# Kernel optimization log

Measured on AMD Instinct MI355X. Metric: run time of the kernel, lower is better.

## Reference

```python
import jax, jax.numpy as jnp
import numpy as np

B, T, D, H, L, W = 32, 512, 256, 8, 2, 10
NQ = 10000
HD = D // H


def setup_inputs():
    key = jax.random.key(0)
    ks = jax.random.split(key, 16)
    def n(k, shape, s=0.02):
        return jax.random.normal(k, shape, jnp.float32) * s
    return {
        "q": jax.random.randint(ks[0], (B, T), 0, NQ),
        "s": jax.random.randint(ks[1], (B, T), 0, 2),
        "q_embed": n(ks[2], (NQ + 1, D)),
        "s_embed": n(ks[3], (2, D)),
        "pos_embed": n(ks[4], (512, D)),
        "fusion_w": n(ks[5], (2 * D, D)),
        "fusion_b": jnp.zeros((D,), jnp.float32),
        "in_proj_w": n(ks[6], (L, D, 3 * D)),
        "in_proj_b": jnp.zeros((L, 3 * D), jnp.float32),
        "out_proj_w": n(ks[7], (L, D, D)),
        "out_proj_b": jnp.zeros((L, D), jnp.float32),
        "ln1_g": jnp.ones((L, D), jnp.float32),
        "ln1_b": jnp.zeros((L, D), jnp.float32),
        "ln2_g": jnp.ones((L, D), jnp.float32),
        "ln2_b": jnp.zeros((L, D), jnp.float32),
        "ff1_w": n(ks[8], (L, D, 4 * D)),
        "ff1_b": jnp.zeros((L, 4 * D), jnp.float32),
        "ff2_w": n(ks[9], (L, 4 * D, D)),
        "ff2_b": jnp.zeros((L, D), jnp.float32),
        "sw1": n(ks[10], (6, 32), 0.1),
        "sb1": jnp.zeros((32,), jnp.float32),
        "sw2": n(ks[11], (32, D // 4), 0.1),
        "sb2": jnp.zeros((D // 4,), jnp.float32),
        "cw1": n(ks[12], (D + D // 4, D)),
        "cb1": jnp.zeros((D,), jnp.float32),
        "cw2": n(ks[13], (D, 1)),
        "cb2": jnp.zeros((1,), jnp.float32),
    }


def _ln(x, g, b):
    mu = jnp.mean(x, -1, keepdims=True)
    var = jnp.mean(jnp.square(x - mu), -1, keepdims=True)
    return (x - mu) * jax.lax.rsqrt(var + 1e-5) * g + b


def _sliding_sum(x, w):
    # sum over trailing window of size w ending at each t, via prefix sums
    c = jnp.concatenate([jnp.zeros((x.shape[0], 1), x.dtype), jnp.cumsum(x, axis=1)], axis=1)
    t = jnp.arange(x.shape[1])
    return c[:, t + 1] - c[:, jnp.maximum(t + 1 - w, 0)]


def _stats(s, mask):
    # vectorized version of _extract_statistics (prefix-sum sliding windows)
    mf = mask.astype(jnp.float32)
    sf = s.astype(jnp.float32) * mf
    valid = _sliding_sum(mf, W)
    correct_rate = _sliding_sum(sf, W) / (valid + 1e-6)
    rc = _sliding_sum(mf, 5)
    recent_correct = _sliding_sum(sf, 5) / (rc + 1e-6)
    trans = ((s[:, 1:] != s[:, :-1]) & mask[:, 1:] & mask[:, :-1]).astype(jnp.float32)
    diff = jnp.concatenate([jnp.zeros((s.shape[0], 1), jnp.float32), trans], axis=1)
    change_rate = _sliding_sum(diff, W - 1) / (valid + 1e-6)
    # max consecutive equal run within each trailing window of size W
    sp = jnp.pad(s, ((0, 0), (W - 1, 0)))
    mp = jnp.pad(mask, ((0, 0), (W - 1, 0)))
    win_s = [sp[:, j:j + T] for j in range(W)]
    win_m = [mp[:, j:j + T] for j in range(W)]
    run = win_m[0].astype(jnp.float32)
    mx = run
    for j in range(1, W):  # fixed small window, not a data-dim loop
        eq = (win_s[j] == win_s[j - 1]) & win_m[j - 1]
        run = win_m[j].astype(jnp.float32) * (jnp.where(eq, run, 0.0) + 1.0)
        mx = jnp.maximum(mx, run)
    rel = jnp.broadcast_to(jnp.arange(T, dtype=jnp.float32) / max(T, 100), s.shape)
    cov = valid / W
    return jnp.stack([correct_rate, recent_correct, change_rate, mx / W, rel, cov], axis=-1)


def reference(q, s, q_embed, s_embed, pos_embed, fusion_w, fusion_b, in_proj_w, in_proj_b,
              out_proj_w, out_proj_b, ln1_g, ln1_b, ln2_g, ln2_b, ff1_w, ff1_b, ff2_w, ff2_b,
              sw1, sb1, sw2, sb2, cw1, cb1, cw2, cb2):
    mask = s >= 0
    qm = jnp.where(mask, q, 0)
    sm = jnp.where(mask, s, 0)
    h = jnp.concatenate([q_embed[qm], s_embed[sm]], axis=-1)  # [B,T,2D]
    h = jax.nn.relu(h @ fusion_w + fusion_b) + pos_embed[:T][None]
    causal = jnp.tril(jnp.ones((T, T), bool))
    allowed = causal[None, None] & mask[:, None, None, :]
    scale = 1.0 / (HD ** 0.5)
    for l in range(L):
        qkv = h @ in_proj_w[l] + in_proj_b[l]
        qh, kh, vh = jnp.split(qkv, 3, axis=-1)
        qh = qh.reshape(B, T, H, HD).transpose(0, 2, 1, 3)
        kh = kh.reshape(B, T, H, HD).transpose(0, 2, 1, 3)
        vh = vh.reshape(B, T, H, HD).transpose(0, 2, 1, 3)
        scores = jnp.einsum('bhqd,bhkd->bhqk', qh, kh) * scale
        scores = jnp.where(allowed, scores, -1e9)
        attn = jax.nn.softmax(scores, axis=-1)
        o = jnp.einsum('bhqk,bhkd->bhqd', attn, vh).transpose(0, 2, 1, 3).reshape(B, T, D)
        h = _ln(h + (o @ out_proj_w[l] + out_proj_b[l]), ln1_g[l], ln1_b[l])
        ff = jax.nn.gelu(h @ ff1_w[l] + ff1_b[l], approximate=False) @ ff2_w[l] + ff2_b[l]
        h = _ln(h + ff, ln2_g[l], ln2_b[l])
    sfeat = _stats(sm, mask)  # [B,T,6]
    semb = jax.nn.relu(sfeat @ sw1 + sb1) @ sw2 + sb2  # [B,T,D//4]
    comb = jnp.concatenate([h, semb], axis=-1)
    logits = (jax.nn.relu(comb @ cw1 + cb1) @ cw2 + cb2)[..., 0]
    return jnp.where(mask, logits, -1e9)
```

## Files before the change

kernel.cpp:

```cpp
#include <hip/hip_runtime.h>
#include <hip/hip_bf16.h>
#include <cmath>


using short8 = __attribute__((ext_vector_type(8))) short;
using short4v = __attribute__((ext_vector_type(4))) short;
using f32x4  = __attribute__((ext_vector_type(4))) float;

__device__ inline float gelu_f(float x) {
    return 0.5f * x * (1.0f + erff(x * 0.70710678118654752f));
}

__device__ inline short f2bf(float x) {
    union { float f; unsigned u; } v; v.f = x;
    return (short)((v.u + 0x7fffu + ((v.u >> 16) & 1u)) >> 16);
}

__device__ inline float bf2f(short v) {
    union { unsigned u; float f; } x; x.u = ((unsigned)(unsigned short)v) << 16;
    return x.f;
}

__device__ inline unsigned packbf(float lo, float hi) {
    union { float f; unsigned u; } a, b; a.f = lo; b.f = hi;
    unsigned ra = (a.u + 0x7fffu + ((a.u >> 16) & 1u)) >> 16;
    unsigned rb = (b.u + 0x7fffu + ((b.u >> 16) & 1u)) >> 16;
    return (rb << 16) | (ra & 0xffffu);
}

#define GLOAD16(gp, lp) __builtin_amdgcn_global_load_lds( \
    (const __attribute__((address_space(1))) void*)(gp), \
    (__attribute__((address_space(3))) void*)(lp), 16, 0, 0)

__global__ __launch_bounds__(256) void prep(
    const float* __restrict__ fusion_w, const float* __restrict__ in_proj_w,
    const float* __restrict__ out_proj_w, const float* __restrict__ ff1_w,
    const float* __restrict__ ff2_w, const float* __restrict__ cw1,
    short* __restrict__ wts,
    const int* __restrict__ s,
    short* __restrict__ semb,
    const float* __restrict__ sw1, const float* __restrict__ sb1,
    const float* __restrict__ sw2, const float* __restrict__ sb2)
{
    __shared__ float tile[32][33];
    __shared__ float sv_sh[512];
    __shared__ float m_sh[512];
    __shared__ float sw2_sh[2048];

    if (blockIdx.x < 1744) {
        const int b0[10]      = {0,128,320,512,576,640,896,1152,1408,1664};
        const int Ks[10]      = {512,256,256,256,256,256,256,1024,1024,320};
        const int Ns[10]      = {256,768,768,256,256,1024,1024,256,256,256};
        const int sidx[10]    = {0,1,1,2,2,3,3,4,4,5};
        const size_t soff[10] = {0,0,196608,0,65536,0,262144,0,262144,0};
        const size_t doff[10] = {0,131072,327680,524288,589824,655360,917504,1179648,1441792,1703936};
        const float* srcs[6] = {fusion_w, in_proj_w, out_proj_w, ff1_w, ff2_w, cw1};
        int bid = blockIdx.x;
        int mi = 0;
        while (mi < 9 && bid >= b0[mi + 1]) ++mi;
        int bl = bid - b0[mi];
        int K = Ks[mi], N = Ns[mi];
        int tx = bl % (N >> 5), ty = bl / (N >> 5);
        const float* src = srcs[sidx[mi]] + soff[mi];
        short* dst = wts + doff[mi];
        int c = threadIdx.x & 31, r = threadIdx.x >> 5;
#pragma unroll
        for (int i = 0; i < 4; ++i)
            tile[r + i * 8][c] = src[(size_t)(ty * 32 + r + i * 8) * N + tx * 32 + c];
        __syncthreads();
#pragma unroll
        for (int i = 0; i < 4; ++i)
            dst[(size_t)(tx * 32 + r + i * 8) * K + ty * 32 + c] = f2bf(tile[c][r + i * 8]);
    } else {
        const int b = blockIdx.x - 1744;
        const int tt = threadIdx.x;
        for (int t = tt; t < 512; t += 256) {
            int sval = s[b * 512 + t];
            bool mk = sval >= 0;
            sv_sh[t] = mk ? (float)sval : 0.f;
            m_sh[t] = mk ? 1.f : 0.f;
        }
        for (int i = tt; i < 2048; i += 256) sw2_sh[i] = sw2[i];
        __syncthreads();
        for (int half = 0; half < 2; ++half) {
            const int t = tt + half * 256;
            float mf10 = 0, sf10 = 0, mf5 = 0, sf5 = 0, d9 = 0;
#pragma unroll
            for (int k = 0; k < 10; ++k) {
                int idx = t - k;
                if (idx >= 0) {
                    float mv = m_sh[idx], sv = sv_sh[idx];
                    mf10 += mv; sf10 += sv;
                    if (k < 5) { mf5 += mv; sf5 += sv; }
                    if (k < 9 && idx >= 1) {
                        if (sv != sv_sh[idx - 1] && mv > 0.5f && m_sh[idx - 1] > 0.5f) d9 += 1.f;
                    }
                }
            }
            float run, mx;
            {
                int x0 = t - 9;
                run = (x0 >= 0) ? m_sh[x0] : 0.f;
                mx = run;
#pragma unroll
                for (int j = 1; j < 10; ++j) {
                    int xc = t + j - 9, xp = xc - 1;
                    float sc = (xc >= 0) ? sv_sh[xc] : 0.f;
                    float sp = (xp >= 0) ? sv_sh[xp] : 0.f;
                    float mc = (xc >= 0) ? m_sh[xc] : 0.f;
                    float mp = (xp >= 0) ? m_sh[xp] : 0.f;
                    bool eq = (sc == sp) && (mp > 0.5f);
                    run = (mc > 0.5f) ? ((eq ? run : 0.f) + 1.f) : 0.f;
                    mx = fmaxf(mx, run);
                }
            }
            float f[6];
            f[0] = sf10 / (mf10 + 1e-6f);
            f[1] = sf5 / (mf5 + 1e-6f);
            f[2] = d9 / (mf10 + 1e-6f);
            f[3] = mx * 0.1f;
            f[4] = (float)t * (1.f / 512.f);
            f[5] = mf10 * 0.1f;

            float hid[32];
#pragma unroll
            for (int j2 = 0; j2 < 32; ++j2) {
                float a = sb1[j2];
#pragma unroll
                for (int i = 0; i < 6; ++i) a = fmaf(f[i], sw1[i * 32 + j2], a);
                hid[j2] = fmaxf(a, 0.f);
            }
            short* orow = semb + ((size_t)b * 512 + t) * 64;
            for (int c = 0; c < 64; c += 4) {
                float v0 = sb2[c], v1 = sb2[c + 1], v2 = sb2[c + 2], v3 = sb2[c + 3];
#pragma unroll
                for (int j2 = 0; j2 < 32; ++j2) {
                    float hh = hid[j2];
                    v0 = fmaf(hh, sw2_sh[j2 * 64 + c], v0);
                    v1 = fmaf(hh, sw2_sh[j2 * 64 + c + 1], v1);
                    v2 = fmaf(hh, sw2_sh[j2 * 64 + c + 2], v2);
                    v3 = fmaf(hh, sw2_sh[j2 * 64 + c + 3], v3);
                }
                short4v o; o[0] = f2bf(v0); o[1] = f2bf(v1); o[2] = f2bf(v2); o[3] = f2bf(v3);
                *(short4v*)(orow + c) = o;
            }
        }
    }
}

template<int EPI, int KTOT>
__global__ __launch_bounds__(512) void kbs(
    const short* __restrict__ A, const short* __restrict__ A2,
    const short* __restrict__ Wt, const float* __restrict__ bias,
    short* __restrict__ o0, short* __restrict__ o1, short* __restrict__ o2,
    short* __restrict__ xbb, short* __restrict__ hb,
    const float* __restrict__ pos, const float* __restrict__ cw2v,
    float* __restrict__ pbuf,
    const int* __restrict__ qi, const int* __restrict__ si,
    const float* __restrict__ qe, const float* __restrict__ se)
{
    constexpr int BN = 64;
    constexpr int NCH = (KTOT + 255) / 256;
    constexpr int KA = (EPI == 4) ? 256 : KTOT;
    __shared__ short Bs[BN * 256];
    const int tid = threadIdx.x, lane = tid & 63, wv = tid >> 6;
    const int lg = lane >> 4, lr = lane & 15;
    const int n0 = blockIdx.y * BN;
    const int row0 = blockIdx.x * 128 + wv * 16;

    f32x4 acc[4] = {};
    short8 af[8];

#pragma unroll
    for (int c = 0; c < NCH; ++c) {
        const int ck = (KTOT - c * 256 >= 256) ? 256 : (KTOT - c * 256);
        const int spr = ck >> 3;
        if (c) __syncthreads();
        for (int i = 0; i < (BN * ck) / 8; i += 512) {
            int slot = i + tid;
            int n = slot / spr, posn = slot % spr;
            int g = posn ^ (n & 7);
            GLOAD16(Wt + (size_t)(n0 + n) * KTOT + c * 256 + g * 8, &Bs[slot * 8]);
        }
        const int nkk = ck >> 5;
        if constexpr (EPI == 0) {
            int row = row0 + lr;
            int sv = si[row];
            bool mk = sv >= 0;
            const float* base = (c == 0) ? qe + (size_t)(mk ? qi[row] : 0) * 256
                                         : se + (size_t)(mk ? sv : 0) * 256;
#pragma unroll
            for (int kk = 0; kk < 8; ++kk) {
                const float* p = base + kk * 32 + lg * 8;
                float4 v0 = *(const float4*)p;
                float4 v1 = *(const float4*)(p + 4);
                short8 o;
                o[0] = f2bf(v0.x); o[1] = f2bf(v0.y); o[2] = f2bf(v0.z); o[3] = f2bf(v0.w);
                o[4] = f2bf(v1.x); o[5] = f2bf(v1.y); o[6] = f2bf(v1.z); o[7] = f2bf(v1.w);
                af[kk] = o;
            }
        } else if (EPI == 4 && c == 1) {
            const short* ar2 = A2 + (size_t)(row0 + lr) * 64 + lg * 8;
            af[0] = *(const short8*)(ar2);
            af[1] = *(const short8*)(ar2 + 32);
        } else {
            const short* ar = A + (size_t)(row0 + lr) * KA + c * 256 + lg * 8;
#pragma unroll
            for (int kk = 0; kk < 8; ++kk)
                if (kk < nkk) af[kk] = *(const short8*)(ar + kk * 32);
        }
        __syncthreads();
#pragma unroll
        for (int kk = 0; kk < 8; ++kk) {
            if (kk >= nkk) break;
#pragma unroll
            for (int j = 0; j < 4; ++j) {
                int n = j * 16 + lr;
                short8 b = *(const short8*)&Bs[n * ck + (((kk * 4 + lg) ^ (n & 7)) << 3)];
                acc[j] = __builtin_amdgcn_mfma_f32_16x16x32_bf16(af[kk], b, acc[j], 0, 0, 0);
            }
        }
    }

    if constexpr (EPI == 0) {
#pragma unroll
        for (int j = 0; j < 4; ++j)
#pragma unroll
        for (int r = 0; r < 4; ++r) {
            int row = row0 + lg * 4 + r;
            int col = n0 + j * 16 + lr;
            float x = acc[j][r] + bias[col];
            x = fmaxf(x, 0.f) + pos[(size_t)(row & 511) * 256 + col];
            o0[(size_t)row * 256 + col] = f2bf(x);
        }
    } else if constexpr (EPI == 1) {
#pragma unroll
        for (int j = 0; j < 4; ++j)
#pragma unroll
        for (int r = 0; r < 4; ++r) {
            int row = row0 + lg * 4 + r;
            int gcol = n0 + j * 16 + lr;
            int t = row & 511, bg = row >> 9;
            int sec = gcol >> 8, cc = gcol & 255;
            int h = cc >> 5, d = cc & 31, bh = bg * 8 + h;
            short v = f2bf(acc[j][r] + bias[gcol]);
            if (sec == 0)      o0[((size_t)bh * 512 + t) * 32 + d] = v;
            else if (sec == 1) o1[((size_t)bh * 512 + t) * 32 + d] = v;
            else {
                int kl = t & 31;
                o2[(size_t)bh * 16384 + (size_t)(t >> 5) * 1024 +
                   (size_t)((kl >> 2) & 3) * 256 + d * 8 + (((kl & 3) << 1) | ((kl >> 4) & 1))] = v;
            }
        }
    } else if constexpr (EPI == 2) {
#pragma unroll
        for (int j = 0; j < 4; ++j)
#pragma unroll
        for (int r = 0; r < 4; ++r) {
            int row = row0 + lg * 4 + r;
            int gcol = n0 + j * 16 + lr;
            float x = acc[j][r] + bias[gcol];
            o0[(size_t)row * 1024 + gcol] = f2bf(gelu_f(x));
        }
    } else if constexpr (EPI == 3) {
#pragma unroll
        for (int j = 0; j < 4; ++j)
#pragma unroll
        for (int r = 0; r < 4; ++r) {
            int row = row0 + lg * 4 + r;
            int col = n0 + j * 16 + lr;
            xbb[(size_t)row * 256 + col] =
                f2bf(acc[j][r] + bias[col] + bf2f(hb[(size_t)row * 256 + col]));
        }
    } else {
#pragma unroll
        for (int r = 0; r < 4; ++r) {
            float p = 0.f;
#pragma unroll
            for (int j = 0; j < 4; ++j) {
                int col = n0 + j * 16 + lr;
                float v = fmaxf(acc[j][r] + bias[col], 0.f);
                p += v * cw2v[col];
            }
#pragma unroll
            for (int off = 1; off < 16; off <<= 1) p += __shfl_xor(p, off);
            if (lr == 0) {
                int row = row0 + lg * 4 + r;
                pbuf[(size_t)blockIdx.y * 16384 + row] = p;
            }
        }
    }
}

__global__ __launch_bounds__(256) void k_ln(
    const short* __restrict__ xbb, short* __restrict__ hb,
    const float* __restrict__ gamma, const float* __restrict__ beta)
{
    int row = blockIdx.x * 4 + (threadIdx.x >> 6);
    int lane = threadIdx.x & 63;
    int c = lane * 4;
    short4v xv4 = *(const short4v*)(xbb + (size_t)row * 256 + c);
    float x0 = bf2f(xv4[0]), x1 = bf2f(xv4[1]), x2 = bf2f(xv4[2]), x3 = bf2f(xv4[3]);
    float sm = x0 + x1 + x2 + x3;
    float sq = x0 * x0 + x1 * x1 + x2 * x2 + x3 * x3;
#pragma unroll
    for (int off = 32; off > 0; off >>= 1) {
        sm += __shfl_xor(sm, off);
        sq += __shfl_xor(sq, off);
    }
    float mu = sm * (1.f / 256.f);
    float var = sq * (1.f / 256.f) - mu * mu;
    float rstd = rsqrtf(var + 1e-5f);
    float4 gv = *reinterpret_cast<const float4*>(gamma + c);
    float4 bv = *reinterpret_cast<const float4*>(beta + c);
    short4v o;
    o[0] = f2bf((x0 - mu) * rstd * gv.x + bv.x);
    o[1] = f2bf((x1 - mu) * rstd * gv.y + bv.y);
    o[2] = f2bf((x2 - mu) * rstd * gv.z + bv.z);
    o[3] = f2bf((x3 - mu) * rstd * gv.w + bv.w);
    *(short4v*)(hb + (size_t)row * 256 + c) = o;
}

__global__ __launch_bounds__(256) void k_fin(
    const float* __restrict__ pbuf, const int* __restrict__ s,
    const float* __restrict__ cb2, float* __restrict__ out)
{
    int i = blockIdx.x * 256 + threadIdx.x;
    float v = pbuf[i] + pbuf[i + 16384] + pbuf[i + 32768] + pbuf[i + 49152] + cb2[0];
    out[i] = (s[i] >= 0) ? v : -1e9f;
}

__global__ __launch_bounds__(256) void attn_mfma(
    const short* __restrict__ Qg, const short* __restrict__ Kg,
    const short* __restrict__ VTg, short* __restrict__ O)
{
    __shared__ unsigned Wp[4][2][16][20];
    const int bh = blockIdx.x >> 2, part = blockIdx.x & 3;
    const int b = bh >> 3, h = bh & 7;
    const int wv = threadIdx.x >> 6, lane = threadIdx.x & 63;
    const int lg = lane >> 4, lr = lane & 15;
    const int slot = part * 4 + wv;
    const short* Qbh = Qg + (size_t)bh * 16384;
    const short* Kbh = Kg + (size_t)bh * 16384;
    const short* Vbh = VTg + (size_t)bh * 16384;
    const float scale = 0.17677669529663687f;

    const int tA = slot, tB = 31 - slot;
    const int qA0 = tA << 4, qB0 = tB << 4;
    const int nA = tA >> 1, nB = tB >> 1;
    short8 qaA = *(const short8*)(Qbh + (size_t)(qA0 + lr) * 32 + lg * 8);
    short8 qaB = *(const short8*)(Qbh + (size_t)(qB0 + lr) * 32 + lg * 8);
    f32x4 oA0 = {}, oA1 = {}, oB0 = {}, oB1 = {};
    float lA[4] = {0.f, 0.f, 0.f, 0.f};
    float lB[4] = {0.f, 0.f, 0.f, 0.f};

    auto chunk = [&](int c, int q0, int nfull, const short8& qa,
                     const short8& kf0, const short8& kf1,
                     const short8& vf0, const short8& vf1,
                     f32x4& o0, f32x4& o1, float* l_, int slab) {
        int kc = c << 5;
        f32x4 s0 = {}, s1 = {};
        s0 = __builtin_amdgcn_mfma_f32_16x16x32_bf16(qa, kf0, s0, 0, 0, 0);
        s1 = __builtin_amdgcn_mfma_f32_16x16x32_bf16(qa, kf1, s1, 0, 0, 0);
        float p0[4], p1[4];
        if (c < nfull) {
#pragma unroll
            for (int r = 0; r < 4; ++r) {
                p0[r] = __expf(s0[r] * scale);
                p1[r] = __expf(s1[r] * scale);
            }
        } else {
#pragma unroll
            for (int r = 0; r < 4; ++r) {
                int qq = q0 + lg * 4 + r;
                p0[r] = (kc + lr)      > qq ? 0.f : __expf(s0[r] * scale);
                p1[r] = (kc + 16 + lr) > qq ? 0.f : __expf(s1[r] * scale);
            }
        }
#pragma unroll
        for (int r = 0; r < 4; ++r) {
            l_[r] += p0[r] + p1[r];
            Wp[wv][slab][lg * 4 + r][lr] = packbf(p0[r], p1[r]);
        }
        short8 pa = *(const short8*)&Wp[wv][slab][lr][lg * 4];
        o0 = __builtin_amdgcn_mfma_f32_16x16x32_bf16(pa, vf0, o0, 0, 0, 0);
        o1 = __builtin_amdgcn_mfma_f32_16x16x32_bf16(pa, vf1, o1, 0, 0, 0);
    };

    int c = 0;
    for (; c <= nA; ++c) {
        int kc = c << 5;
        short8 kf0 = *(const short8*)(Kbh + (size_t)(kc + lr) * 32 + lg * 8);
        short8 kf1 = *(const short8*)(Kbh + (size_t)(kc + 16 + lr) * 32 + lg * 8);
        short8 vf0 = *(const short8*)(Vbh + (size_t)c * 1024 + lg * 256 + lr * 8);
        short8 vf1 = *(const short8*)(Vbh + (size_t)c * 1024 + lg * 256 + (lr + 16) * 8);
        chunk(c, qB0, nB, qaB, kf0, kf1, vf0, vf1, oB0, oB1, lB, 1);
        chunk(c, qA0, nA, qaA, kf0, kf1, vf0, vf1, oA0, oA1, lA, 0);
    }
    for (; c <= nB; ++c) {
        int kc = c << 5;
        short8 kf0 = *(const short8*)(Kbh + (size_t)(kc + lr) * 32 + lg * 8);
        short8 kf1 = *(const short8*)(Kbh + (size_t)(kc + 16 + lr) * 32 + lg * 8);
        short8 vf0 = *(const short8*)(Vbh + (size_t)c * 1024 + lg * 256 + lr * 8);
        short8 vf1 = *(const short8*)(Vbh + (size_t)c * 1024 + lg * 256 + (lr + 16) * 8);
        chunk(c, qB0, nB, qaB, kf0, kf1, vf0, vf1, oB0, oB1, lB, 1);
    }

#pragma unroll
    for (int off = 1; off < 16; off <<= 1)
#pragma unroll
        for (int r = 0; r < 4; ++r) {
            lA[r] += __shfl_xor(lA[r], off);
            lB[r] += __shfl_xor(lB[r], off);
        }
#pragma unroll
    for (int r = 0; r < 4; ++r) {
        float invA = 1.f / lA[r];
        size_t roA = ((size_t)b * 512 + qA0 + lg * 4 + r) * 256 + h * 32;
        O[roA + lr] = f2bf(oA0[r] * invA);
        O[roA + 16 + lr] = f2bf(oA1[r] * invA);
        float invB = 1.f / lB[r];
        size_t roB = ((size_t)b * 512 + qB0 + lg * 4 + r) * 256 + h * 32;
        O[roB + lr] = f2bf(oB0[r] * invB);
        O[roB + 16 + lr] = f2bf(oB1[r] * invB);
    }
}

extern "C" void kernel_launch(void* const* d_in, const int* in_sizes, int n_in,
                              void* d_out, int out_size, void* d_ws, size_t ws_size,
                              hipStream_t stream) {
    const int*   q         = (const int*)d_in[0];
    const int*   s         = (const int*)d_in[1];
    const float* q_embed   = (const float*)d_in[2];
    const float* s_embed   = (const float*)d_in[3];
    const float* pos_embed = (const float*)d_in[4];
    const float* fusion_w  = (const float*)d_in[5];
    const float* fusion_b  = (const float*)d_in[6];
    const float* in_proj_w = (const float*)d_in[7];
    const float* in_proj_b = (const float*)d_in[8];
    const float* out_proj_w= (const float*)d_in[9];
    const float* out_proj_b= (const float*)d_in[10];
    const float* ln1_g     = (const float*)d_in[11];
    const float* ln1_b     = (const float*)d_in[12];
    const float* ln2_g     = (const float*)d_in[13];
    const float* ln2_b     = (const float*)d_in[14];
    const float* ff1_w     = (const float*)d_in[15];
    const float* ff1_b     = (const float*)d_in[16];
    const float* ff2_w     = (const float*)d_in[17];
    const float* ff2_b     = (const float*)d_in[18];
    const float* sw1       = (const float*)d_in[19];
    const float* sb1       = (const float*)d_in[20];
    const float* sw2       = (const float*)d_in[21];
    const float* sb2       = (const float*)d_in[22];
    const float* cw1       = (const float*)d_in[23];
    const float* cb1       = (const float*)d_in[24];
    const float* cw2       = (const float*)d_in[25];
    const float* cb2       = (const float*)d_in[26];
    float* out = (float*)d_out;

    char* base = (char*)d_ws;
    short* hb   = (short*)(base);
    short* bufA = (short*)(base + 8388608);
    short* att  = (short*)(base + 41943040);
    short* Qg   = (short*)(base + 50331648);
    short* Kg   = (short*)(base + 58720256);
    short* VTg  = (short*)(base + 67108864);
    short* semb = (short*)(base + 75497472);
    short* wts  = (short*)(base + 77594624);
    short* xbb  = (short*)(base + 81166336);
    float* pbuf = (float*)(base + 89554944);

    const size_t W_FUSION = 0, W_INPROJ0 = 131072, W_INPROJ1 = 327680;
    const size_t W_OUTPROJ0 = 524288, W_OUTPROJ1 = 589824;
    const size_t W_FF1_0 = 655360, W_FF1_1 = 917504;
    const size_t W_FF2_0 = 1179648, W_FF2_1 = 1441792;
    const size_t W_CW1 = 1703936;

    prep<<<1776, 256, 0, stream>>>(fusion_w, in_proj_w, out_proj_w,
                                   ff1_w, ff2_w, cw1, wts,
                                   s, semb, sw1, sb1, sw2, sb2);
    kbs<0, 512><<<dim3(128, 4), 512, 0, stream>>>(nullptr, nullptr,
        wts + W_FUSION, fusion_b, hb, nullptr, nullptr, nullptr, nullptr,
        pos_embed, nullptr, nullptr, q, s, q_embed, s_embed);
    for (int l = 0; l < 2; ++l) {
        kbs<1, 256><<<dim3(128, 12), 512, 0, stream>>>(hb, nullptr,
            wts + (l ? W_INPROJ1 : W_INPROJ0), in_proj_b + l * 768,
            Qg, Kg, VTg, nullptr, nullptr, nullptr, nullptr, nullptr,
            nullptr, nullptr, nullptr, nullptr);
        attn_mfma<<<1024, 256, 0, stream>>>(Qg, Kg, VTg, att);
        kbs<3, 256><<<dim3(128, 4), 512, 0, stream>>>(att, nullptr,
            wts + (l ? W_OUTPROJ1 : W_OUTPROJ0), out_proj_b + l * 256,
            nullptr, nullptr, nullptr, xbb, hb, nullptr, nullptr, nullptr,
            nullptr, nullptr, nullptr, nullptr);
        k_ln<<<4096, 256, 0, stream>>>(xbb, hb, ln1_g + l * 256, ln1_b + l * 256);
        kbs<2, 256><<<dim3(128, 16), 512, 0, stream>>>(hb, nullptr,
            wts + (l ? W_FF1_1 : W_FF1_0), ff1_b + l * 1024,
            bufA, nullptr, nullptr, nullptr, nullptr, nullptr, nullptr, nullptr,
            nullptr, nullptr, nullptr, nullptr);
        kbs<3, 1024><<<dim3(128, 4), 512, 0, stream>>>(bufA, nullptr,
            wts + (l ? W_FF2_1 : W_FF2_0), ff2_b + l * 256,
            nullptr, nullptr, nullptr, xbb, hb, nullptr, nullptr, nullptr,
            nullptr, nullptr, nullptr, nullptr);
        k_ln<<<4096, 256, 0, stream>>>(xbb, hb, ln2_g + l * 256, ln2_b + l * 256);
    }
    kbs<4, 320><<<dim3(128, 4), 512, 0, stream>>>(hb, semb,
        wts + W_CW1, cb1, nullptr, nullptr, nullptr, nullptr, nullptr,
        nullptr, cw2, pbuf, nullptr, nullptr, nullptr, nullptr);
    k_fin<<<64, 256, 0, stream>>>(pbuf, s, cb2, out);
}
```

Baseline: 285.0 us.

## Fuse residual GEMMs with LayerNorm and classifier head into full-width kernels

Adds a kfull kernel in which each block computes all 256 output columns for 32 rows, so the residual add and LayerNorm can run in the GEMM epilogue through a cross-wave shared-memory reduction. This replaces the out-proj and FF2 GEMMs followed by separate k_ln launches, and also folds the classifier reduction and final masking into the head GEMM, removing k_fin and the xbb/pbuf intermediates. It removes several launches and round trips of intermediates through global memory. In exchange the grid shrinks to 512 blocks, and each block now stages the whole 256-column weight slab through shared memory in 128-wide K chunks.

```diff
diff --git a/kernel.cpp b/kernel.cpp
--- a/kernel.cpp
+++ b/kernel.cpp
@@ -150,18 +150,15 @@
 
 template<int EPI, int KTOT>
 __global__ __launch_bounds__(512) void kbs(
-    const short* __restrict__ A, const short* __restrict__ A2,
-    const short* __restrict__ Wt, const float* __restrict__ bias,
+    const short* __restrict__ A, const short* __restrict__ Wt,
+    const float* __restrict__ bias,
     short* __restrict__ o0, short* __restrict__ o1, short* __restrict__ o2,
-    short* __restrict__ xbb, short* __restrict__ hb,
-    const float* __restrict__ pos, const float* __restrict__ cw2v,
-    float* __restrict__ pbuf,
+    const float* __restrict__ pos,
     const int* __restrict__ qi, const int* __restrict__ si,
     const float* __restrict__ qe, const float* __restrict__ se)
 {
     constexpr int BN = 64;
     constexpr int NCH = (KTOT + 255) / 256;
-    constexpr int KA = (EPI == 4) ? 256 : KTOT;
     __shared__ short Bs[BN * 256];
     const int tid = threadIdx.x, lane = tid & 63, wv = tid >> 6;
     const int lg = lane >> 4, lr = lane & 15;
@@ -199,12 +196,8 @@
                 o[4] = f2bf(v1.x); o[5] = f2bf(v1.y); o[6] = f2bf(v1.z); o[7] = f2bf(v1.w);
                 af[kk] = o;
             }
-        } else if (EPI == 4 && c == 1) {
-            const short* ar2 = A2 + (size_t)(row0 + lr) * 64 + lg * 8;
-            af[0] = *(const short8*)(ar2);
-            af[1] = *(const short8*)(ar2 + 32);
         } else {
-            const short* ar = A + (size_t)(row0 + lr) * KA + c * 256 + lg * 8;
+            const short* ar = A + (size_t)(row0 + lr) * KTOT + c * 256 + lg * 8;
 #pragma unroll
             for (int kk = 0; kk < 8; ++kk)
                 if (kk < nkk) af[kk] = *(const short8*)(ar + kk * 32);
@@ -252,7 +245,7 @@
                    (size_t)((kl >> 2) & 3) * 256 + d * 8 + (((kl & 3) << 1) | ((kl >> 4) & 1))] = v;
             }
         }
-    } else if constexpr (EPI == 2) {
+    } else {
 #pragma unroll
         for (int j = 0; j < 4; ++j)
 #pragma unroll
@@ -262,72 +255,135 @@
             float x = acc[j][r] + bias[gcol];
             o0[(size_t)row * 1024 + gcol] = f2bf(gelu_f(x));
         }
-    } else if constexpr (EPI == 3) {
+    }
+}
+
+template<int EPI, int KTOT>
+__global__ __launch_bounds__(512) void kfull(
+    const short* __restrict__ A, const short* __restrict__ A2,
+    const short* __restrict__ Wt, const float* __restrict__ bias,
+    short* __restrict__ hb,
+    const float* __restrict__ gamma, const float* __restrict__ beta,
+    const float* __restrict__ cw2v, const float* __restrict__ cb2,
+    const int* __restrict__ smask, float* __restrict__ outlog)
+{
+    constexpr int NCH = (KTOT + 127) / 128;
+    constexpr int KA = (EPI == 1) ? 256 : KTOT;
+    __shared__ short Bs[256 * 128];
+    __shared__ float redS[32][4];
+    __shared__ float redQ[32][4];
+    const int tid = threadIdx.x, lane = tid & 63, wv = tid >> 6;
+    const int lg = lane >> 4, lr = lane & 15;
+    const int wr = wv >> 2, wc = wv & 3;
+    const int row0 = blockIdx.x * 32 + wr * 16;
+
+    f32x4 acc[4] = {};
+    short8 af[4];
+
+#pragma unroll
+    for (int c = 0; c < NCH; ++c) {
+        const int ck = (KTOT - c * 128 >= 128) ? 128 : (KTOT - c * 128);
+        const int spr = ck >> 3;
+        if (c) __syncthreads();
+        for (int i = 0; i < (256 * ck) / 8; i += 512) {
+            int slot = i + tid;
+            int n = slot / spr, posn = slot % spr;
+            int g = posn ^ (n & 7);
+            GLOAD16(Wt + (size_t)n * KTOT + c * 128 + g * 8, &Bs[slot * 8]);
+        }
+        const int nkk = ck >> 5;
+        if (EPI == 1 && c == 2) {
+            const short* ar2 = A2 + (size_t)(row0 + lr) * 64 + lg * 8;
+            af[0] = *(const short8*)(ar2);
+            af[1] = *(const short8*)(ar2 + 32);
+        } else {
+            const short* ar = A + (size_t)(row0 + lr) * KA + c * 128 + lg * 8;
+#pragma unroll
+            for (int kk = 0; kk < 4; ++kk)
+                if (kk < nkk) af[kk] = *(const short8*)(ar + kk * 32);
+        }
+        __syncthreads();
+#pragma unroll
+        for (int kk = 0; kk < 4; ++kk) {
+            if (kk >= nkk) break;
+#pragma unroll
+            for (int j = 0; j < 4; ++j) {
+                int n = wc * 64 + j * 16 + lr;
+                short8 b = *(const short8*)&Bs[n * ck + (((kk * 4 + lg) ^ (n & 7)) << 3)];
+                acc[j] = __builtin_amdgcn_mfma_f32_16x16x32_bf16(af[kk], b, acc[j], 0, 0, 0);
+            }
+        }
+    }
+
+    if constexpr (EPI == 0) {
+        float ps[4] = {0.f, 0.f, 0.f, 0.f}, pq[4] = {0.f, 0.f, 0.f, 0.f};
 #pragma unroll
         for (int j = 0; j < 4; ++j)
 #pragma unroll
         for (int r = 0; r < 4; ++r) {
             int row = row0 + lg * 4 + r;
-            int col = n0 + j * 16 + lr;
-            xbb[(size_t)row * 256 + col] =
-                f2bf(acc[j][r] + bias[col] + bf2f(hb[(size_t)row * 256 + col]));
+            int col = wc * 64 + j * 16 + lr;
+            float x = acc[j][r] + bias[col] + bf2f(hb[(size_t)row * 256 + col]);
+            acc[j][r] = x;
+            ps[r] += x; pq[r] += x * x;
+        }
+#pragma unroll
+        for (int off = 1; off < 16; off <<= 1)
+#pragma unroll
+            for (int r = 0; r < 4; ++r) {
+                ps[r] += __shfl_xor(ps[r], off);
+                pq[r] += __shfl_xor(pq[r], off);
+            }
+        if (lr == 0) {
+#pragma unroll
+            for (int r = 0; r < 4; ++r) {
+                int rl = wr * 16 + lg * 4 + r;
+                redS[rl][wc] = ps[r]; redQ[rl][wc] = pq[r];
+            }
+        }
+        __syncthreads();
+#pragma unroll
+        for (int r = 0; r < 4; ++r) {
+            int rl = wr * 16 + lg * 4 + r;
+            int row = row0 + lg * 4 + r;
+            float sm = redS[rl][0] + redS[rl][1] + redS[rl][2] + redS[rl][3];
+            float sq = redQ[rl][0] + redQ[rl][1] + redQ[rl][2] + redQ[rl][3];
+            float mu = sm * (1.f / 256.f);
+            float var = sq * (1.f / 256.f) - mu * mu;
+            float rstd = rsqrtf(var + 1e-5f);
+#pragma unroll
+            for (int j = 0; j < 4; ++j) {
+                int col = wc * 64 + j * 16 + lr;
+                float y = (acc[j][r] - mu) * rstd * gamma[col] + beta[col];
+                hb[(size_t)row * 256 + col] = f2bf(y);
+            }
         }
     } else {
-#pragma unroll
-        for (int r = 0; r < 4; ++r) {
-            float p = 0.f;
-#pragma unroll
-            for (int j = 0; j < 4; ++j) {
-                int col = n0 + j * 16 + lr;
-                float v = fmaxf(acc[j][r] + bias[col], 0.f);
-                p += v * cw2v[col];
-            }
-#pragma unroll
-            for (int off = 1; off < 16; off <<= 1) p += __shfl_xor(p, off);
-            if (lr == 0) {
-                int row = row0 + lg * 4 + r;
-                pbuf[(size_t)blockIdx.y * 16384 + row] = p;
-            }
-        }
-    }
-}
-
-__global__ __launch_bounds__(256) void k_ln(
-    const short* __restrict__ xbb, short* __restrict__ hb,
-    const float* __restrict__ gamma, const float* __restrict__ beta)
-{
-    int row = blockIdx.x * 4 + (threadIdx.x >> 6);
-    int lane = threadIdx.x & 63;
-    int c = lane * 4;
-    short4v xv4 = *(const short4v*)(xbb + (size_t)row * 256 + c);
-    float x0 = bf2f(xv4[0]), x1 = bf2f(xv4[1]), x2 = bf2f(xv4[2]), x3 = bf2f(xv4[3]);
-    float sm = x0 + x1 + x2 + x3;
-    float sq = x0 * x0 + x1 * x1 + x2 * x2 + x3 * x3;
-#pragma unroll
-    for (int off = 32; off > 0; off >>= 1) {
-        sm += __shfl_xor(sm, off);
-        sq += __shfl_xor(sq, off);
-    }
-    float mu = sm * (1.f / 256.f);
-    float var = sq * (1.f / 256.f) - mu * mu;
-    float rstd = rsqrtf(var + 1e-5f);
-    float4 gv = *reinterpret_cast<const float4*>(gamma + c);
-    float4 bv = *reinterpret_cast<const float4*>(beta + c);
-    short4v o;
-    o[0] = f2bf((x0 - mu) * rstd * gv.x + bv.x);
-    o[1] = f2bf((x1 - mu) * rstd * gv.y + bv.y);
-    o[2] = f2bf((x2 - mu) * rstd * gv.z + bv.z);
-    o[3] = f2bf((x3 - mu) * rstd * gv.w + bv.w);
-    *(short4v*)(hb + (size_t)row * 256 + c) = o;
-}
-
-__global__ __launch_bounds__(256) void k_fin(
-    const float* __restrict__ pbuf, const int* __restrict__ s,
-    const float* __restrict__ cb2, float* __restrict__ out)
-{
-    int i = blockIdx.x * 256 + threadIdx.x;
-    float v = pbuf[i] + pbuf[i + 16384] + pbuf[i + 32768] + pbuf[i + 49152] + cb2[0];
-    out[i] = (s[i] >= 0) ? v : -1e9f;
+        float p[4] = {0.f, 0.f, 0.f, 0.f};
+#pragma unroll
+        for (int j = 0; j < 4; ++j)
+#pragma unroll
+        for (int r = 0; r < 4; ++r) {
+            int col = wc * 64 + j * 16 + lr;
+            float v = fmaxf(acc[j][r] + bias[col], 0.f);
+            p[r] += v * cw2v[col];
+        }
+#pragma unroll
+        for (int off = 1; off < 16; off <<= 1)
+#pragma unroll
+            for (int r = 0; r < 4; ++r) p[r] += __shfl_xor(p[r], off);
+        if (lr == 0) {
+#pragma unroll
+            for (int r = 0; r < 4; ++r)
+                redS[wr * 16 + lg * 4 + r][wc] = p[r];
+        }
+        __syncthreads();
+        if (tid < 32) {
+            int row = blockIdx.x * 32 + tid;
+            float v = redS[tid][0] + redS[tid][1] + redS[tid][2] + redS[tid][3] + cb2[0];
+            outlog[row] = (smask[row] >= 0) ? v : -1e9f;
+        }
+    }
 }
 
 __global__ __launch_bounds__(256) void attn_mfma(
@@ -467,8 +523,6 @@
     short* VTg  = (short*)(base + 67108864);
     short* semb = (short*)(base + 75497472);
     short* wts  = (short*)(base + 77594624);
-    short* xbb  = (short*)(base + 81166336);
-    float* pbuf = (float*)(base + 89554944);
 
     const size_t W_FUSION = 0, W_INPROJ0 = 131072, W_INPROJ1 = 327680;
     const size_t W_OUTPROJ0 = 524288, W_OUTPROJ1 = 589824;
@@ -479,32 +533,27 @@
     prep<<<1776, 256, 0, stream>>>(fusion_w, in_proj_w, out_proj_w,
                                    ff1_w, ff2_w, cw1, wts,
                                    s, semb, sw1, sb1, sw2, sb2);
-    kbs<0, 512><<<dim3(128, 4), 512, 0, stream>>>(nullptr, nullptr,
-        wts + W_FUSION, fusion_b, hb, nullptr, nullptr, nullptr, nullptr,
-        pos_embed, nullptr, nullptr, q, s, q_embed, s_embed);
+    kbs<0, 512><<<dim3(128, 4), 512, 0, stream>>>(nullptr,
+        wts + W_FUSION, fusion_b, hb, nullptr, nullptr,
+        pos_embed, q, s, q_embed, s_embed);
     for (int l = 0; l < 2; ++l) {
-        kbs<1, 256><<<dim3(128, 12), 512, 0, stream>>>(hb, nullptr,
+        kbs<1, 256><<<dim3(128, 12), 512, 0, stream>>>(hb,
             wts + (l ? W_INPROJ1 : W_INPROJ0), in_proj_b + l * 768,
-            Qg, Kg, VTg, nullptr, nullptr, nullptr, nullptr, nullptr,
+            Qg, Kg, VTg, nullptr, nullptr, nullptr, nullptr, nullptr);
+        attn_mfma<<<1024, 256, 0, stream>>>(Qg, Kg, VTg, att);
+        kfull<0, 256><<<512, 512, 0, stream>>>(att, nullptr,
+            wts + (l ? W_OUTPROJ1 : W_OUTPROJ0), out_proj_b + l * 256,
+            hb, ln1_g + l * 256, ln1_b + l * 256,
             nullptr, nullptr, nullptr, nullptr);
-        attn_mfma<<<1024, 256, 0, stream>>>(Qg, Kg, VTg, att);
-        kbs<3, 256><<<dim3(128, 4), 512, 0, stream>>>(att, nullptr,
-            wts + (l ? W_OUTPROJ1 : W_OUTPROJ0), out_proj_b + l * 256,
-            nullptr, nullptr, nullptr, xbb, hb, nullptr, nullptr, nullptr,
+        kbs<2, 256><<<dim3(128, 16), 512, 0, stream>>>(hb,
+            wts + (l ? W_FF1_1 : W_FF1_0), ff1_b + l * 1024,
+            bufA, nullptr, nullptr, nullptr, nullptr, nullptr, nullptr, nullptr);
+        kfull<0, 1024><<<512, 512, 0, stream>>>(bufA, nullptr,
+            wts + (l ? W_FF2_1 : W_FF2_0), ff2_b + l * 256,
+            hb, ln2_g + l * 256, ln2_b + l * 256,
             nullptr, nullptr, nullptr, nullptr);
-        k_ln<<<4096, 256, 0, stream>>>(xbb, hb, ln1_g + l * 256, ln1_b + l * 256);
-        kbs<2, 256><<<dim3(128, 16), 512, 0, stream>>>(hb, nullptr,
-            wts + (l ? W_FF1_1 : W_FF1_0), ff1_b + l * 1024,
-            bufA, nullptr, nullptr, nullptr, nullptr, nullptr, nullptr, nullptr,
-            nullptr, nullptr, nullptr, nullptr);
-        kbs<3, 1024><<<dim3(128, 4), 512, 0, stream>>>(bufA, nullptr,
-            wts + (l ? W_FF2_1 : W_FF2_0), ff2_b + l * 256,
-            nullptr, nullptr, nullptr, xbb, hb, nullptr, nullptr, nullptr,
-            nullptr, nullptr, nullptr, nullptr);
-        k_ln<<<4096, 256, 0, stream>>>(xbb, hb, ln2_g + l * 256, ln2_b + l * 256);
-    }
-    kbs<4, 320><<<dim3(128, 4), 512, 0, stream>>>(hb, semb,
-        wts + W_CW1, cb1, nullptr, nullptr, nullptr, nullptr, nullptr,
-        nullptr, cw2, pbuf, nullptr, nullptr, nullptr, nullptr);
-    k_fin<<<64, 256, 0, stream>>>(pbuf, s, cb2, out);
-}
+    }
+    kfull<1, 320><<<512, 512, 0, stream>>>(hb, semb,
+        wts + W_CW1, cb1, nullptr, nullptr, nullptr,
+        cw2, cb2, s, out);
+}
```

Result: no change. 280.8 us (-1.4%).
